# Optimization experiments

Hardware: AMD Instinct MI355X
Metric: run time of the kernel (lower is better)

## Reference

```python
import jax, jax.numpy as jnp
import numpy as np

B, S, E, H = 2, 2048, 1024, 16
D = E // H  # head_dim = 64
SCALE = D ** -0.5


def setup_inputs() -> dict:
    key = jax.random.key(0)
    ks = jax.random.split(key, 5)
    std = E ** -0.5
    return {
        "x": jax.random.normal(ks[0], (B, S, E), dtype=jnp.float32),
        "wq": jax.random.normal(ks[1], (E, E), dtype=jnp.float32) * std,
        "wk": jax.random.normal(ks[2], (E, E), dtype=jnp.float32) * std,
        "wv": jax.random.normal(ks[3], (E, E), dtype=jnp.float32) * std,
        "wo": jax.random.normal(ks[4], (E, E), dtype=jnp.float32) * std,
    }


def reference(x, wq, wk, wv, wo):
    b, s, e = x.shape
    # nn.Linear(bias=False): y = x @ W.T; then split heads -> [B,H,S,D]
    def heads(w):
        return jnp.einsum('bse,fe->bsf', x, w).reshape(b, s, H, D).transpose(0, 2, 1, 3)
    q, k, v = heads(wq), heads(wk), heads(wv)
    attn = jnp.einsum('bhqd,bhkd->bhqk', q, k) * SCALE  # [B,H,S,S]
    attn = jax.nn.softmax(attn, axis=-1)
    out = jnp.einsum('bhqk,bhkd->bhqd', attn, v)        # [B,H,S,D]
    out = out.transpose(0, 2, 1, 3).reshape(b, s, e)
    return jnp.einsum('bse,fe->bsf', out, wo)
```

## Files before the change

### kernel.cpp

```cpp
#include <hip/hip_runtime.h>
#include <stdint.h>

typedef unsigned short ushort_t;
typedef __bf16 bfx8 __attribute__((ext_vector_type(8), may_alias));
typedef __bf16 bfx2 __attribute__((ext_vector_type(2), may_alias));
typedef unsigned short usx8 __attribute__((ext_vector_type(8), may_alias));
typedef unsigned int uix2 __attribute__((ext_vector_type(2), may_alias));
typedef unsigned int uix4 __attribute__((ext_vector_type(4), may_alias));
typedef float f32x2 __attribute__((ext_vector_type(2)));
typedef float f32x4 __attribute__((ext_vector_type(4)));
typedef float f32x4m __attribute__((ext_vector_type(4), may_alias));
typedef float f32x16 __attribute__((ext_vector_type(16)));

#define BB 2
#define SS 2048
#define EE 1024
#define HH 16
#define DD 64
#define MM (BB * SS)
#define XN ((size_t)MM * EE)
#define WN ((size_t)EE * EE)
#define QSCALE 0.18033688011112042f

__device__ __forceinline__ unsigned short f2bf(float f) {
  unsigned int u = __builtin_bit_cast(unsigned int, f);
  u += 0x7fffu + ((u >> 16) & 1u);
  return (unsigned short)(u >> 16);
}

__device__ __forceinline__ usx8 cvt8(const float* p) {
  f32x4m a = *(const f32x4m*)p;
  f32x4m b = *(const f32x4m*)(p + 4);
  usx8 r;
  r[0] = f2bf(a[0]); r[1] = f2bf(a[1]); r[2] = f2bf(a[2]); r[3] = f2bf(a[3]);
  r[4] = f2bf(b[0]); r[5] = f2bf(b[1]); r[6] = f2bf(b[2]); r[7] = f2bf(b[3]);
  return r;
}

__device__ __forceinline__ unsigned int pk2(float lo, float hi) {
  bfx2 t;
  t[0] = (__bf16)lo;
  t[1] = (__bf16)hi;
  return __builtin_bit_cast(unsigned int, t);
}

__device__ __forceinline__ void gl_lds16(const ushort_t* g, ushort_t* l) {
  __builtin_amdgcn_global_load_lds(
      (const __attribute__((address_space(1))) unsigned int*)g,
      (__attribute__((address_space(3))) unsigned int*)l, 16, 0, 0);
}

__global__ __launch_bounds__(256)
void cvt_qkv(const float* __restrict__ x, const float* __restrict__ wq,
             const float* __restrict__ wk, const float* __restrict__ wv,
             ushort_t* __restrict__ dst) {
  size_t i8 = ((size_t)blockIdx.x * 256 + threadIdx.x) * 8;
  const float* s;
  size_t off;
  if (i8 < XN)               { s = x;  off = i8; }
  else if (i8 < XN + WN)     { s = wq; off = i8 - XN; }
  else if (i8 < XN + 2 * WN) { s = wk; off = i8 - XN - WN; }
  else                       { s = wv; off = i8 - XN - 2 * WN; }
  *(usx8*)(dst + i8) = cvt8(s + off);
}

__global__ __launch_bounds__(256)
void cvt_one(const float* __restrict__ s, ushort_t* __restrict__ dst) {
  size_t i8 = ((size_t)blockIdx.x * 256 + threadIdx.x) * 8;
  *(usx8*)(dst + i8) = cvt8(s + i8);
}

__global__ __launch_bounds__(256)
void gemm_qkv(const ushort_t* __restrict__ xb,
              const ushort_t* __restrict__ wqb, const ushort_t* __restrict__ wkb,
              const ushort_t* __restrict__ wvb,
              ushort_t* __restrict__ Qb, ushort_t* __restrict__ Kb,
              ushort_t* __restrict__ Vtb) {
  __shared__ ushort_t As[128 * 32];
  __shared__ ushort_t Bs[128 * 32];

  const int bid = blockIdx.x;
  const ushort_t *A, *W;
  ushort_t* C;
  int bx, by, N;
  float scale = 1.0f;
  if (bid < 512) {
    int t = bid & 255;
    bx = t & 7;  by = t >> 3;
    A = xb;  N = EE;
    if (bid < 256) { W = wqb; C = Qb; scale = QSCALE; }
    else           { W = wkb; C = Kb; }
  } else {
    int t = bid - 512;
    bx = t & 31; by = t >> 5;
    A = wvb; W = xb; C = Vtb; N = MM;
  }
  const int K = EE;

  const int tid = threadIdx.x;
  const int lane = tid & 63;
  const int w = tid >> 6;
  const int l15 = lane & 15, l16 = lane >> 4;
  const int m0 = by * 128;
  const int n0 = bx * 128;
  const int wr = w >> 1, wc = w & 1;

  f32x4 acc[4][4];
#pragma unroll
  for (int i = 0; i < 4; ++i)
#pragma unroll
    for (int j = 0; j < 4; ++j)
#pragma unroll
      for (int r = 0; r < 4; ++r) acc[i][j][r] = 0.0f;

  for (int k0 = 0; k0 < K; k0 += 32) {
#pragma unroll
    for (int q = 0; q < 2; ++q) {
      int c = w * 128 + q * 64 + lane;
      int row = c >> 2, col = c & 3;
      gl_lds16(A + (size_t)(m0 + row) * K + k0 + col * 8,
               As + (size_t)(w * 128 + q * 64) * 8);
      gl_lds16(W + (size_t)(n0 + row) * K + k0 + col * 8,
               Bs + (size_t)(w * 128 + q * 64) * 8);
    }
    __syncthreads();

    bfx8 af[4], bfr[4];
#pragma unroll
    for (int i = 0; i < 4; ++i) {
      int mr = wr * 64 + i * 16 + l15;
      af[i] = *(const bfx8*)(As + mr * 32 + l16 * 8);
      int nr = wc * 64 + i * 16 + l15;
      bfr[i] = *(const bfx8*)(Bs + nr * 32 + l16 * 8);
    }
#pragma unroll
    for (int i = 0; i < 4; ++i)
#pragma unroll
      for (int j = 0; j < 4; ++j)
        acc[i][j] = __builtin_amdgcn_mfma_f32_16x16x32_bf16(af[i], bfr[j],
                                                            acc[i][j], 0, 0, 0);
    __syncthreads();
  }

#pragma unroll
  for (int i = 0; i < 4; ++i) {
    int mr = m0 + wr * 64 + i * 16 + l16 * 4;
#pragma unroll
    for (int j = 0; j < 4; ++j) {
      int nc = n0 + wc * 64 + j * 16 + l15;
#pragma unroll
      for (int r = 0; r < 4; ++r)
        C[(size_t)(mr + r) * N + nc] = f2bf(acc[i][j][r] * scale);
    }
  }
}

__global__ __launch_bounds__(256)
void gemm_o(const ushort_t* __restrict__ A, const ushort_t* __restrict__ W,
            float* __restrict__ C, int M, int N, int K) {
  __shared__ ushort_t As[64 * 32];
  __shared__ ushort_t Bs[128 * 32];

  const int tid = threadIdx.x;
  const int lane = tid & 63;
  const int w = tid >> 6;
  const int l15 = lane & 15, l16 = lane >> 4;
  const int m0 = blockIdx.y * 64;
  const int n0 = blockIdx.x * 128;
  const int wr = w >> 1, wc = w & 1;

  f32x4 acc[2][4];
#pragma unroll
  for (int i = 0; i < 2; ++i)
#pragma unroll
    for (int j = 0; j < 4; ++j)
#pragma unroll
      for (int r = 0; r < 4; ++r) acc[i][j][r] = 0.0f;

  const int ca = w * 64 + lane;
  const int ar = ca >> 2, ac = ca & 3;

  for (int k0 = 0; k0 < K; k0 += 32) {
    gl_lds16(A + (size_t)(m0 + ar) * K + k0 + ac * 8,
             As + (size_t)(w * 64) * 8);
#pragma unroll
    for (int q = 0; q < 2; ++q) {
      int c = w * 128 + q * 64 + lane;
      int row = c >> 2, col = c & 3;
      gl_lds16(W + (size_t)(n0 + row) * K + k0 + col * 8,
               Bs + (size_t)(w * 128 + q * 64) * 8);
    }
    __syncthreads();

    bfx8 af[2], bfr[4];
#pragma unroll
    for (int i = 0; i < 2; ++i) {
      int mr = wr * 32 + i * 16 + l15;
      af[i] = *(const bfx8*)(As + mr * 32 + l16 * 8);
    }
#pragma unroll
    for (int j = 0; j < 4; ++j) {
      int nr = wc * 64 + j * 16 + l15;
      bfr[j] = *(const bfx8*)(Bs + nr * 32 + l16 * 8);
    }
#pragma unroll
    for (int i = 0; i < 2; ++i)
#pragma unroll
      for (int j = 0; j < 4; ++j)
        acc[i][j] = __builtin_amdgcn_mfma_f32_16x16x32_bf16(af[i], bfr[j],
                                                            acc[i][j], 0, 0, 0);
    __syncthreads();
  }

#pragma unroll
  for (int i = 0; i < 2; ++i) {
    int mr = m0 + wr * 32 + i * 16 + l16 * 4;
#pragma unroll
    for (int j = 0; j < 4; ++j) {
      int nc = n0 + wc * 64 + j * 16 + l15;
#pragma unroll
      for (int r = 0; r < 4; ++r)
        C[(size_t)(mr + r) * N + nc] = acc[i][j][r];
    }
  }
}

__global__ __launch_bounds__(256)
void attn_fwd(const ushort_t* Q, const ushort_t* __restrict__ Kg,
              const ushort_t* __restrict__ Vt_g, ushort_t* AO) {
  __shared__ ushort_t Ks0[64 * 72];
  __shared__ ushort_t Vs0[64 * 72];
  __shared__ ushort_t Ks1[64 * 72];
  __shared__ ushort_t Vs1[64 * 72];

  const int tid = threadIdx.x;
  const int lane = tid & 63;
  const int w = tid >> 6;
  const int l31 = lane & 31, hi = lane >> 5;
  const int n = blockIdx.x;
  const int xcd = n & 7, rr = n >> 3;
  const int g = xcd * 4 + (rr >> 4);
  const int qt = rr & 15;
  const int h = g & 15, b = g >> 4;
  const int q0 = qt * 128 + w * 32;

  const ushort_t* kbase = Kg + (size_t)b * SS * EE + h * DD;
  const ushort_t* vbase = Vt_g + (size_t)h * DD * MM + (size_t)b * SS;

  bfx8 bq[4];
#pragma unroll
  for (int t = 0; t < 4; ++t)
    bq[t] = *(const bfx8*)(Q + (size_t)(b * SS + q0 + l31) * EE + h * DD +
                           t * 16 + hi * 8);

  f32x16 o0, o1;
#pragma unroll
  for (int r = 0; r < 16; ++r) { o0[r] = 0.0f; o1[r] = 0.0f; }
  f32x2 ls2;
  ls2[0] = 0.0f; ls2[1] = 0.0f;

  const int r0 = tid >> 3, c0 = tid & 7;

  usx8 k0r, k1r, v0r, v1r;
  auto load_t = [&](int key0) {
    k0r = *(const usx8*)(kbase + (size_t)(key0 + r0) * EE + c0 * 8);
    k1r = *(const usx8*)(kbase + (size_t)(key0 + r0 + 32) * EE + c0 * 8);
    v0r = *(const usx8*)(vbase + (size_t)r0 * MM + key0 + c0 * 8);
    v1r = *(const usx8*)(vbase + (size_t)(r0 + 32) * MM + key0 + c0 * 8);
  };
  auto write_t = [&](ushort_t* Ksb, ushort_t* Vsb) {
    *(usx8*)(Ksb + r0 * 72 + c0 * 8) = k0r;
    *(usx8*)(Ksb + (r0 + 32) * 72 + c0 * 8) = k1r;
    *(usx8*)(Vsb + r0 * 72 + c0 * 8) = v0r;
    *(usx8*)(Vsb + (r0 + 32) * 72 + c0 * 8) = v1r;
  };
  auto compute_t = [&](const ushort_t* Ksb, const ushort_t* Vsb) {
    f32x16 pa, pb;
#pragma unroll
    for (int r = 0; r < 16; ++r) { pa[r] = 0.0f; pb[r] = 0.0f; }
    __builtin_amdgcn_s_setprio(1);
#pragma unroll
    for (int t = 0; t < 4; ++t) {
      bfx8 ak0 = *(const bfx8*)(Ksb + l31 * 72 + t * 16 + hi * 8);
      bfx8 ak1 = *(const bfx8*)(Ksb + (32 + l31) * 72 + t * 16 + hi * 8);
      pa = __builtin_amdgcn_mfma_f32_32x32x16_bf16(ak0, bq[t], pa, 0, 0, 0);
      pb = __builtin_amdgcn_mfma_f32_32x32x16_bf16(ak1, bq[t], pb, 0, 0, 0);
    }
    __builtin_amdgcn_s_setprio(0);

#pragma unroll
    for (int r = 0; r < 16; ++r) {
      pa[r] = __builtin_exp2f(pa[r]);
      pb[r] = __builtin_exp2f(pb[r]);
    }
#pragma unroll
    for (int s = 0; s < 8; ++s) {
      f32x2 ta, tb;
      ta[0] = pa[2 * s]; ta[1] = pa[2 * s + 1];
      tb[0] = pb[2 * s]; tb[1] = pb[2 * s + 1];
      ls2 += ta + tb;
    }

    unsigned int dwA[8], dwB[8];
#pragma unroll
    for (int s = 0; s < 8; ++s) {
      dwA[s] = pk2(pa[2 * s], pa[2 * s + 1]);
      dwB[s] = pk2(pb[2 * s], pb[2 * s + 1]);
    }
    bfx8 fd[4];
#pragma unroll
    for (int g2 = 0; g2 < 2; ++g2) {
      auto sA = __builtin_amdgcn_permlane32_swap(dwA[4 * g2 + 0],
                                                 dwA[4 * g2 + 2], false, false);
      auto sB = __builtin_amdgcn_permlane32_swap(dwA[4 * g2 + 1],
                                                 dwA[4 * g2 + 3], false, false);
      uix4 f;
      f[0] = sA[0]; f[1] = sB[0]; f[2] = sA[1]; f[3] = sB[1];
      fd[g2] = __builtin_bit_cast(bfx8, f);
      auto tA = __builtin_amdgcn_permlane32_swap(dwB[4 * g2 + 0],
                                                 dwB[4 * g2 + 2], false, false);
      auto tB = __builtin_amdgcn_permlane32_swap(dwB[4 * g2 + 1],
                                                 dwB[4 * g2 + 3], false, false);
      uix4 f2;
      f2[0] = tA[0]; f2[1] = tB[0]; f2[2] = tA[1]; f2[3] = tB[1];
      fd[2 + g2] = __builtin_bit_cast(bfx8, f2);
    }

    __builtin_amdgcn_s_setprio(1);
#pragma unroll
    for (int kk = 0; kk < 4; ++kk) {
      bfx8 av0 = *(const bfx8*)(Vsb + l31 * 72 + kk * 16 + hi * 8);
      bfx8 av1 = *(const bfx8*)(Vsb + (32 + l31) * 72 + kk * 16 + hi * 8);
      o0 = __builtin_amdgcn_mfma_f32_32x32x16_bf16(av0, fd[kk], o0, 0, 0, 0);
      o1 = __builtin_amdgcn_mfma_f32_32x32x16_bf16(av1, fd[kk], o1, 0, 0, 0);
    }
    __builtin_amdgcn_s_setprio(0);
  };

  load_t(0);
  write_t(Ks0, Vs0);
  __syncthreads();

  for (int kt = 0; kt < SS; kt += 128) {
    load_t(kt + 64);
    compute_t(Ks0, Vs0);
    write_t(Ks1, Vs1);
    __syncthreads();
    if (kt + 128 < SS) load_t(kt + 128);
    compute_t(Ks1, Vs1);
    if (kt + 128 < SS) {
      write_t(Ks0, Vs0);
      __syncthreads();
    }
  }

  float lsum = ls2[0] + ls2[1];
  lsum += __shfl_xor(lsum, 32);
  float inv = 1.0f / lsum;

  ushort_t* orow = AO + (size_t)(b * SS + q0 + l31) * EE + h * DD;
#pragma unroll
  for (int g2 = 0; g2 < 4; ++g2) {
    uix2 s0, s1;
    s0[0] = pk2(o0[4 * g2 + 0] * inv, o0[4 * g2 + 1] * inv);
    s0[1] = pk2(o0[4 * g2 + 2] * inv, o0[4 * g2 + 3] * inv);
    *(uix2*)(orow + 8 * g2 + 4 * hi) = s0;
    s1[0] = pk2(o1[4 * g2 + 0] * inv, o1[4 * g2 + 1] * inv);
    s1[1] = pk2(o1[4 * g2 + 2] * inv, o1[4 * g2 + 3] * inv);
    *(uix2*)(orow + 32 + 8 * g2 + 4 * hi) = s1;
  }
}

extern "C" void kernel_launch(void* const* d_in, const int* in_sizes, int n_in,
                              void* d_out, int out_size, void* d_ws, size_t ws_size,
                              hipStream_t stream) {
  const float* x  = (const float*)d_in[0];
  const float* wq = (const float*)d_in[1];
  const float* wk = (const float*)d_in[2];
  const float* wv = (const float*)d_in[3];
  const float* wo = (const float*)d_in[4];
  float* out = (float*)d_out;

  ushort_t* Qb  = (ushort_t*)d_ws;
  ushort_t* Kb  = Qb + XN;
  ushort_t* Vtb = Kb + XN;
  ushort_t* Ab  = Qb;
  ushort_t* S    = (ushort_t*)d_out;
  ushort_t* xb   = S;
  ushort_t* wqb  = S + XN;
  ushort_t* wkb  = S + XN + WN;
  ushort_t* wvb  = S + XN + 2 * WN;
  ushort_t* wob  = Kb;

  dim3 blk(256);
  cvt_qkv<<<dim3((unsigned)((XN + 3 * WN) / (256 * 8))), blk, 0, stream>>>(
      x, wq, wk, wv, S);
  gemm_qkv<<<dim3(768), blk, 0, stream>>>(xb, wqb, wkb, wvb, Qb, Kb, Vtb);
  attn_fwd<<<dim3(512), blk, 0, stream>>>(Qb, Kb, Vtb, Ab);
  cvt_one<<<dim3((unsigned)(WN / (256 * 8))), blk, 0, stream>>>(wo, wob);
  gemm_o<<<dim3(EE / 128, MM / 64), blk, 0, stream>>>(
      Ab, wob, out, MM, EE, EE);
}
```

Measured before the change: 197.6 us.

## Split attention key range across two wave groups per block and merge

The attention kernel now launches 512 threads per block. Two groups of four waves each process half of the key sequence, with their own double-buffered K/V LDS tiles. Partial outputs and row sums are merged through LDS, and the second group normalizes and writes the result. This raises the number of waves in flight and halves each block's serial key loop. In exchange it doubles LDS per block, adds a reduction step, and under the 512-thread launch bound may limit registers per thread.

```diff
diff --git a/kernel.cpp b/kernel.cpp
--- a/kernel.cpp
+++ b/kernel.cpp
@@ -225,24 +225,30 @@
   }
 }
 
-__global__ __launch_bounds__(256)
+__global__ __launch_bounds__(512)
 void attn_fwd(const ushort_t* Q, const ushort_t* __restrict__ Kg,
               const ushort_t* __restrict__ Vt_g, ushort_t* AO) {
-  __shared__ ushort_t Ks0[64 * 72];
-  __shared__ ushort_t Vs0[64 * 72];
-  __shared__ ushort_t Ks1[64 * 72];
-  __shared__ ushort_t Vs1[64 * 72];
+  __shared__ ushort_t KV[2 * 4 * 4608];
 
   const int tid = threadIdx.x;
   const int lane = tid & 63;
   const int w = tid >> 6;
+  const int half = w >> 2;
+  const int wq = w & 3;
   const int l31 = lane & 31, hi = lane >> 5;
   const int n = blockIdx.x;
   const int xcd = n & 7, rr = n >> 3;
   const int g = xcd * 4 + (rr >> 4);
   const int qt = rr & 15;
   const int h = g & 15, b = g >> 4;
-  const int q0 = qt * 128 + w * 32;
+  const int q0 = qt * 128 + wq * 32;
+  const int kOff = half * (SS / 2);
+
+  ushort_t* Hb = KV + half * 4 * 4608;
+  ushort_t* Ks0 = Hb;
+  ushort_t* Vs0 = Hb + 4608;
+  ushort_t* Ks1 = Hb + 2 * 4608;
+  ushort_t* Vs1 = Hb + 3 * 4608;
 
   const ushort_t* kbase = Kg + (size_t)b * SS * EE + h * DD;
   const ushort_t* vbase = Vt_g + (size_t)h * DD * MM + (size_t)b * SS;
@@ -259,7 +265,8 @@
   f32x2 ls2;
   ls2[0] = 0.0f; ls2[1] = 0.0f;
 
-  const int r0 = tid >> 3, c0 = tid & 7;
+  const int ht = tid & 255;
+  const int r0 = ht >> 3, c0 = ht & 7;
 
   usx8 k0r, k1r, v0r, v1r;
   auto load_t = [&](int key0) {
@@ -337,37 +344,57 @@
     __builtin_amdgcn_s_setprio(0);
   };
 
-  load_t(0);
+  load_t(kOff);
   write_t(Ks0, Vs0);
   __syncthreads();
 
-  for (int kt = 0; kt < SS; kt += 128) {
-    load_t(kt + 64);
+  for (int kt = 0; kt < SS / 2; kt += 128) {
+    load_t(kOff + kt + 64);
     compute_t(Ks0, Vs0);
     write_t(Ks1, Vs1);
     __syncthreads();
-    if (kt + 128 < SS) load_t(kt + 128);
+    if (kt + 128 < SS / 2) load_t(kOff + kt + 128);
     compute_t(Ks1, Vs1);
-    if (kt + 128 < SS) {
+    if (kt + 128 < SS / 2) {
       write_t(Ks0, Vs0);
       __syncthreads();
     }
   }
 
   float lsum = ls2[0] + ls2[1];
-  lsum += __shfl_xor(lsum, 32);
-  float inv = 1.0f / lsum;
-
-  ushort_t* orow = AO + (size_t)(b * SS + q0 + l31) * EE + h * DD;
-#pragma unroll
-  for (int g2 = 0; g2 < 4; ++g2) {
-    uix2 s0, s1;
-    s0[0] = pk2(o0[4 * g2 + 0] * inv, o0[4 * g2 + 1] * inv);
-    s0[1] = pk2(o0[4 * g2 + 2] * inv, o0[4 * g2 + 3] * inv);
-    *(uix2*)(orow + 8 * g2 + 4 * hi) = s0;
-    s1[0] = pk2(o1[4 * g2 + 0] * inv, o1[4 * g2 + 1] * inv);
-    s1[1] = pk2(o1[4 * g2 + 2] * inv, o1[4 * g2 + 3] * inv);
-    *(uix2*)(orow + 32 + 8 * g2 + 4 * hi) = s1;
+
+  float* mbuf = (float*)KV + (size_t)(w & 3) * 64 * 33;
+  __syncthreads();
+  if (half == 0) {
+#pragma unroll
+    for (int r = 0; r < 16; ++r) {
+      mbuf[lane * 33 + r] = o0[r];
+      mbuf[lane * 33 + 16 + r] = o1[r];
+    }
+    mbuf[lane * 33 + 32] = lsum;
+  }
+  __syncthreads();
+  if (half == 1) {
+#pragma unroll
+    for (int r = 0; r < 16; ++r) {
+      o0[r] += mbuf[lane * 33 + r];
+      o1[r] += mbuf[lane * 33 + 16 + r];
+    }
+    lsum += mbuf[lane * 33 + 32];
+    lsum += __shfl_xor(lsum, 32);
+    float inv = 1.0f / lsum;
+
+    ushort_t* orow = AO + (size_t)(b * SS + q0 + l31) * EE + h * DD;
+#pragma unroll
+    for (int g2 = 0; g2 < 4; ++g2) {
+      uix2 s0, s1;
+      s0[0] = pk2(o0[4 * g2 + 0] * inv, o0[4 * g2 + 1] * inv);
+      s0[1] = pk2(o0[4 * g2 + 2] * inv, o0[4 * g2 + 3] * inv);
+      *(uix2*)(orow + 8 * g2 + 4 * hi) = s0;
+      s1[0] = pk2(o1[4 * g2 + 0] * inv, o1[4 * g2 + 1] * inv);
+      s1[1] = pk2(o1[4 * g2 + 2] * inv, o1[4 * g2 + 3] * inv);
+      *(uix2*)(orow + 32 + 8 * g2 + 4 * hi) = s1;
+    }
   }
 }
 
@@ -396,7 +423,7 @@
   cvt_qkv<<<dim3((unsigned)((XN + 3 * WN) / (256 * 8))), blk, 0, stream>>>(
       x, wq, wk, wv, S);
   gemm_qkv<<<dim3(768), blk, 0, stream>>>(xb, wqb, wkb, wvb, Qb, Kb, Vtb);
-  attn_fwd<<<dim3(512), blk, 0, stream>>>(Qb, Kb, Vtb, Ab);
+  attn_fwd<<<dim3(512), dim3(512), 0, stream>>>(Qb, Kb, Vtb, Ab);
   cvt_one<<<dim3((unsigned)(WN / (256 * 8))), blk, 0, stream>>>(wo, wob);
   gemm_o<<<dim3(EE / 128, MM / 64), blk, 0, stream>>>(
       Ab, wob, out, MM, EE, EE);
```

Result: no change. 200.9 us (+1.6%).

## Remap GEMM tile order per XCD and simplify attention load addressing

Applied to the files above, without the earlier changes.

Block indices in the QKV and output projection GEMMs are remapped so that blocks landing on the same XCD (round-robin by block id mod 8) share A-row tiles, which should improve L2 reuse. The output GEMM moves to a 1-D grid to support this. In attention, the K/V load pointers are now incremented in place rather than recomputed from the key offset, and the first QK MFMA takes a hoisted zero accumulator instead of re-zeroing it every tile. The remap assumes an 8-XCD round-robin dispatch and exact grid shapes.

```diff
diff --git a/kernel.cpp b/kernel.cpp
--- a/kernel.cpp
+++ b/kernel.cpp
@@ -86,13 +86,17 @@
   float scale = 1.0f;
   if (bid < 512) {
     int t = bid & 255;
-    bx = t & 7;  by = t >> 3;
+    int xcd = t & 7, p = t >> 3;
+    by = xcd * 4 + (p >> 3);
+    bx = p & 7;
     A = xb;  N = EE;
     if (bid < 256) { W = wqb; C = Qb; scale = QSCALE; }
     else           { W = wkb; C = Kb; }
   } else {
     int t = bid - 512;
-    bx = t & 31; by = t >> 5;
+    int xcd = t & 7, p = t >> 3;
+    by = xcd;
+    bx = p;
     A = wvb; W = xb; C = Vtb; N = MM;
   }
   const int K = EE;
@@ -161,12 +165,17 @@
   __shared__ ushort_t As[64 * 32];
   __shared__ ushort_t Bs[128 * 32];
 
+  const int n = blockIdx.x;
+  const int xcd = n & 7, p = n >> 3;
+  const int by = xcd * 8 + (p >> 3);
+  const int bx = p & 7;
+
   const int tid = threadIdx.x;
   const int lane = tid & 63;
   const int w = tid >> 6;
   const int l15 = lane & 15, l16 = lane >> 4;
-  const int m0 = blockIdx.y * 64;
-  const int n0 = blockIdx.x * 128;
+  const int m0 = by * 64;
+  const int n0 = bx * 128;
   const int wr = w >> 1, wc = w & 1;
 
   f32x4 acc[2][4];
@@ -259,14 +268,27 @@
   f32x2 ls2;
   ls2[0] = 0.0f; ls2[1] = 0.0f;
 
+  f32x16 z16;
+#pragma unroll
+  for (int r = 0; r < 16; ++r) z16[r] = 0.0f;
+
   const int r0 = tid >> 3, c0 = tid & 7;
 
+  const ushort_t* kpA = kbase + (size_t)r0 * EE + c0 * 8;
+  const ushort_t* kpB = kbase + (size_t)(r0 + 32) * EE + c0 * 8;
+  const ushort_t* vpA = vbase + (size_t)r0 * MM + c0 * 8;
+  const ushort_t* vpB = vbase + (size_t)(r0 + 32) * MM + c0 * 8;
+
   usx8 k0r, k1r, v0r, v1r;
-  auto load_t = [&](int key0) {
-    k0r = *(const usx8*)(kbase + (size_t)(key0 + r0) * EE + c0 * 8);
-    k1r = *(const usx8*)(kbase + (size_t)(key0 + r0 + 32) * EE + c0 * 8);
-    v0r = *(const usx8*)(vbase + (size_t)r0 * MM + key0 + c0 * 8);
-    v1r = *(const usx8*)(vbase + (size_t)(r0 + 32) * MM + key0 + c0 * 8);
+  auto load_t = [&]() {
+    k0r = *(const usx8*)kpA;
+    k1r = *(const usx8*)kpB;
+    v0r = *(const usx8*)vpA;
+    v1r = *(const usx8*)vpB;
+    kpA += (size_t)64 * EE;
+    kpB += (size_t)64 * EE;
+    vpA += 64;
+    vpB += 64;
   };
   auto write_t = [&](ushort_t* Ksb, ushort_t* Vsb) {
     *(usx8*)(Ksb + r0 * 72 + c0 * 8) = k0r;
@@ -276,11 +298,15 @@
   };
   auto compute_t = [&](const ushort_t* Ksb, const ushort_t* Vsb) {
     f32x16 pa, pb;
-#pragma unroll
-    for (int r = 0; r < 16; ++r) { pa[r] = 0.0f; pb[r] = 0.0f; }
     __builtin_amdgcn_s_setprio(1);
-#pragma unroll
-    for (int t = 0; t < 4; ++t) {
+    {
+      bfx8 ak0 = *(const bfx8*)(Ksb + l31 * 72 + hi * 8);
+      bfx8 ak1 = *(const bfx8*)(Ksb + (32 + l31) * 72 + hi * 8);
+      pa = __builtin_amdgcn_mfma_f32_32x32x16_bf16(ak0, bq[0], z16, 0, 0, 0);
+      pb = __builtin_amdgcn_mfma_f32_32x32x16_bf16(ak1, bq[0], z16, 0, 0, 0);
+    }
+#pragma unroll
+    for (int t = 1; t < 4; ++t) {
       bfx8 ak0 = *(const bfx8*)(Ksb + l31 * 72 + t * 16 + hi * 8);
       bfx8 ak1 = *(const bfx8*)(Ksb + (32 + l31) * 72 + t * 16 + hi * 8);
       pa = __builtin_amdgcn_mfma_f32_32x32x16_bf16(ak0, bq[t], pa, 0, 0, 0);
@@ -337,16 +363,16 @@
     __builtin_amdgcn_s_setprio(0);
   };
 
-  load_t(0);
+  load_t();
   write_t(Ks0, Vs0);
   __syncthreads();
 
   for (int kt = 0; kt < SS; kt += 128) {
-    load_t(kt + 64);
+    load_t();
     compute_t(Ks0, Vs0);
     write_t(Ks1, Vs1);
     __syncthreads();
-    if (kt + 128 < SS) load_t(kt + 128);
+    if (kt + 128 < SS) load_t();
     compute_t(Ks1, Vs1);
     if (kt + 128 < SS) {
       write_t(Ks0, Vs0);
@@ -398,6 +424,6 @@
   gemm_qkv<<<dim3(768), blk, 0, stream>>>(xb, wqb, wkb, wvb, Qb, Kb, Vtb);
   attn_fwd<<<dim3(512), blk, 0, stream>>>(Qb, Kb, Vtb, Ab);
   cvt_one<<<dim3((unsigned)(WN / (256 * 8))), blk, 0, stream>>>(wo, wob);
-  gemm_o<<<dim3(EE / 128, MM / 64), blk, 0, stream>>>(
+  gemm_o<<<dim3(512), blk, 0, stream>>>(
       Ab, wob, out, MM, EE, EE);
 }
```

Measured after the change: 196.1 us. No clear change (-0.8%).
